# Optimization experiments

Measured on AMD Instinct MI355X. Metric: run time of the kernel, lower is better.

The kernel has to match this reference:

```python
import jax, jax.numpy as jnp
import numpy as np

B, IN_DIM, HID = 4096, 1024, 1024


def setup_inputs() -> dict:
    key = jax.random.key(0)
    ks = jax.random.split(key, 6)
    x_t = jax.random.normal(ks[0], (B, IN_DIM), dtype=jnp.float32)
    h_prev = jax.random.normal(ks[1], (B, HID), dtype=jnp.float32)
    c_prev = jax.random.normal(ks[2], (B, HID), dtype=jnp.float32)
    # stacked input-proj weights for gates (f, i, o, g): [4H, in_dim]
    U_w = jax.random.normal(ks[3], (4 * HID, IN_DIM), dtype=jnp.float32) * (1.0 / np.sqrt(IN_DIM))
    # biases: zeros except forget-gate bias = 1.0 (matches Uf.bias.fill_(1.0))
    U_b = jnp.concatenate([jnp.ones((HID,), jnp.float32), jnp.zeros((3 * HID,), jnp.float32)])
    # stacked hidden-proj weights (no bias): [4H, H]
    W_w = jax.random.normal(ks[4], (4 * HID, HID), dtype=jnp.float32) * (1.0 / np.sqrt(HID))
    return {"x_t": x_t, "h_prev": h_prev, "c_prev": c_prev,
            "U_w": U_w, "U_b": U_b, "W_w": W_w}


def reference(x_t, h_prev, c_prev, U_w, U_b, W_w):
    # two concatenated GEMMs covering all 8 original Linear layers
    pre = x_t @ U_w.T + U_b + h_prev @ W_w.T  # [B, 4H]
    f_pre, i_pre, o_pre, g_pre = jnp.split(pre, 4, axis=-1)
    f_t = jax.nn.sigmoid(f_pre)
    i_t = jax.nn.sigmoid(i_pre)
    o_t = jax.nn.sigmoid(o_pre)
    g_t = jnp.tanh(g_pre)
    c_t = f_t * c_prev + i_t * g_t
    h_t = o_t * jnp.tanh(c_t)
    return (h_t, c_t)
```

## Files before the change

### kernel.cpp

```cpp
#include <hip/hip_runtime.h>
#include <hip/hip_bf16.h>


#define BATCH 4096
#define HID   1024
#define KDIM  2048

#define BM 256
#define BN 256
#define BK 64
#define NITER (KDIM / (2 * BK))

typedef __bf16 bf16x8 __attribute__((ext_vector_type(8)));
typedef float  f32x4  __attribute__((ext_vector_type(4)));

__device__ __forceinline__ void async_load16(const void* g, void* l) {
    __builtin_amdgcn_global_load_lds(
        (const __attribute__((address_space(1))) void*)g,
        (__attribute__((address_space(3))) void*)l,
        16, 0, 0);
}

__device__ __forceinline__ float sigmoidf_(float v) {
    return 1.0f / (1.0f + __expf(-v));
}
__device__ __forceinline__ float tanhf_(float v) {
    return 1.0f - 2.0f / (__expf(2.0f * v) + 1.0f);
}

__global__ __launch_bounds__(256) void convert_kernel(
    const float* __restrict__ x, const float* __restrict__ h,
    const float* __restrict__ U, const float* __restrict__ W,
    __hip_bfloat16* __restrict__ Acat, __hip_bfloat16* __restrict__ Bcat)
{
    const int CH_PER_MAT = (4096 * KDIM) / 8;
    int idx = blockIdx.x * blockDim.x + threadIdx.x;
    bool isB = idx >= CH_PER_MAT;
    int c = isB ? (idx - CH_PER_MAT) : idx;
    int row  = c >> 8;
    int col  = (c & 255) << 3;
    int srow = row;
    if (isB) {
        int g  = (row >> 4) & 3;
        int j  = ((row >> 8) << 6) + (((row >> 6) & 3) << 4) + (row & 15);
        srow = g * 1024 + j;
    }
    const float* src;
    if (col < 1024) src = (isB ? U : x) + (size_t)srow * 1024 + col;
    else            src = (isB ? W : h) + (size_t)srow * 1024 + (col - 1024);
    float4 v0 = *(const float4*)(src);
    float4 v1 = *(const float4*)(src + 4);
    __hip_bfloat16 tmp[8];
    tmp[0] = __float2bfloat16(v0.x); tmp[1] = __float2bfloat16(v0.y);
    tmp[2] = __float2bfloat16(v0.z); tmp[3] = __float2bfloat16(v0.w);
    tmp[4] = __float2bfloat16(v1.x); tmp[5] = __float2bfloat16(v1.y);
    tmp[6] = __float2bfloat16(v1.z); tmp[7] = __float2bfloat16(v1.w);
    __hip_bfloat16* dst = (isB ? Bcat : Acat) + (size_t)row * KDIM + col;
    *(bf16x8*)dst = *(const bf16x8*)tmp;
}

__global__ __launch_bounds__(512, 1) void gemm_lstm_kernel(
    const __hip_bfloat16* __restrict__ A,
    const __hip_bfloat16* __restrict__ Bm,
    const float* __restrict__ Ub,
    const float* __restrict__ c_prev,
    float* __restrict__ out)
{
    __shared__ __align__(16) unsigned char smem[131072];

    const int tid  = threadIdx.x;
    const int lane = tid & 63;
    const int wid  = tid >> 6;
    const int wm   = wid >> 2;
    const int wn   = wid & 3;

    int wg  = blockIdx.x;
    const int xcd = wg & 7;
    const int i_  = wg >> 3;
    const int bm = ((xcd >> 1) << 2) + (i_ >> 3);
    const int bn = ((xcd & 1) << 3) + (i_ & 7);

    const __hip_bfloat16* Ab = A  + (size_t)bm * BM * KDIM;
    const __hip_bfloat16* Bb = Bm + (size_t)bn * BN * KDIM;

    const int frow = lane & 15;
    const int kq   = lane >> 4;
    const int esw  = (frow >> 1) & 7;
    const unsigned xs0 = (unsigned)((kq ^ esw) << 4);
    const unsigned xs1 = xs0 ^ 64u;
    const unsigned wmBase = (unsigned)wm * 16384u;
    const unsigned bnBase = (unsigned)(wn >> 1) * 16384u;
    const unsigned bnRow  = (unsigned)(wn & 1) * 64u;

    const int ch0 = tid,           ch1 = 512 + tid;
    const int sr0 = ch0 >> 3,      sr1 = ch1 >> 3;
    const int sc0 = ((ch0 & 7) ^ ((sr0 >> 1) & 7)) << 3;
    const int sc1 = ((ch1 & 7) ^ ((sr1 >> 1) & 7)) << 3;
    const size_t ga0 = (size_t)sr0 * KDIM + sc0;
    const size_t ga1 = (size_t)sr1 * KDIM + sc1;

    f32x4 acc[8][4] = {};
    bf16x8 arE[4], arO[4], brE[4], brO[4];

#define RD16(B) (*(const bf16x8*)(smem + (B)))
#define LDA4(SET, BUFB, MH, XS) do { \
    const unsigned _b = (BUFB) + wmBase; \
    SET[0] = RD16(_b + (unsigned)((MH)*64 +  0 + frow)*128u + (XS)); \
    SET[1] = RD16(_b + (unsigned)((MH)*64 + 16 + frow)*128u + (XS)); \
    SET[2] = RD16(_b + (unsigned)((MH)*64 + 32 + frow)*128u + (XS)); \
    SET[3] = RD16(_b + (unsigned)((MH)*64 + 48 + frow)*128u + (XS)); } while (0)
#define LDB4(SET, BUFB, XS) do { \
    const unsigned _b = (BUFB) + 32768u + bnBase; \
    SET[0] = RD16(_b + (bnRow +  0 + frow)*128u + (XS)); \
    SET[1] = RD16(_b + (bnRow + 16 + frow)*128u + (XS)); \
    SET[2] = RD16(_b + (bnRow + 32 + frow)*128u + (XS)); \
    SET[3] = RD16(_b + (bnRow + 48 + frow)*128u + (XS)); } while (0)
#define STG_A(TSRC, BUFB, H) do { \
    const unsigned _rg = (BUFB) + (H)*16384u; \
    const __hip_bfloat16* _s = Ab + (size_t)(H)*128*KDIM + (size_t)(TSRC)*64; \
    async_load16(_s + ga0, smem + _rg + (unsigned)ch0*16u); \
    async_load16(_s + ga1, smem + _rg + (unsigned)ch1*16u); } while (0)
#define STG_B(TSRC, BUFB, H) do { \
    const unsigned _rg = (BUFB) + 32768u + (H)*16384u; \
    const __hip_bfloat16* _s = Bb + (size_t)(H)*128*KDIM + (size_t)(TSRC)*64; \
    async_load16(_s + ga0, smem + _rg + (unsigned)ch0*16u); \
    async_load16(_s + ga1, smem + _rg + (unsigned)ch1*16u); } while (0)
#define MF16(ASET, BSET, MB) do { \
    __builtin_amdgcn_s_setprio(1); \
    _Pragma("unroll") for (int _m = 0; _m < 4; ++_m) \
    _Pragma("unroll") for (int _n = 0; _n < 4; ++_n) \
        acc[(MB)+_m][_n] = __builtin_amdgcn_mfma_f32_16x16x32_bf16( \
            ASET[_m], BSET[_n], acc[(MB)+_m][_n], 0, 0, 0); \
    __builtin_amdgcn_s_setprio(0); } while (0)
#define DRAIN_LGKM asm volatile("s_waitcnt lgkmcnt(0)" ::: "memory")
#define WAIT_VM4   asm volatile("s_waitcnt vmcnt(4)" ::: "memory")
#define PH_BAR __builtin_amdgcn_s_barrier()

    STG_B(0, 0u, 0); STG_B(0, 0u, 1);
    STG_A(0, 0u, 0); STG_A(0, 0u, 1);
    STG_B(1, 65536u, 0); STG_B(1, 65536u, 1);
    STG_A(1, 65536u, 0);
    asm volatile("s_waitcnt vmcnt(6)" ::: "memory");
    PH_BAR;
    LDA4(arE, 0u, 0, xs0); LDB4(brE, 0u, xs0);

#pragma unroll 1
    for (int i = 0; i < NITER; ++i) {
        const int tb = 2 * i + 1;
        const int tc = (2 * i + 2 < 32) ? 2 * i + 2 : 31;
        const int td = (2 * i + 3 < 32) ? 2 * i + 3 : 31;

        LDA4(arO, 0u, 0, xs1); LDB4(brO, 0u, xs1);
        STG_A(tb, 65536u, 1);
        MF16(arE, brE, 0);
        DRAIN_LGKM; PH_BAR;
        LDA4(arE, 0u, 1, xs0);
        STG_B(tc, 0u, 0);
        MF16(arO, brO, 0);
        PH_BAR;
        LDA4(arO, 0u, 1, xs1);
        STG_B(tc, 0u, 1);
        MF16(arE, brE, 4);
        DRAIN_LGKM; WAIT_VM4; PH_BAR;
        LDA4(arE, 65536u, 0, xs0); LDB4(brE, 65536u, xs0);
        STG_A(tc, 0u, 0);
        MF16(arO, brO, 4);
        PH_BAR;
        LDA4(arO, 65536u, 0, xs1); LDB4(brO, 65536u, xs1);
        STG_A(tc, 0u, 1);
        MF16(arE, brE, 0);
        DRAIN_LGKM; PH_BAR;
        LDA4(arE, 65536u, 1, xs0);
        STG_B(td, 65536u, 0);
        MF16(arO, brO, 0);
        PH_BAR;
        LDA4(arO, 65536u, 1, xs1);
        STG_B(td, 65536u, 1);
        MF16(arE, brE, 4);
        DRAIN_LGKM; WAIT_VM4; PH_BAR;
        LDA4(arE, 0u, 0, xs0); LDB4(brE, 0u, xs0);
        STG_A(td, 65536u, 0);
        MF16(arO, brO, 4);
        PH_BAR;
    }
#undef RD16
#undef LDA4
#undef LDB4
#undef STG_A
#undef STG_B
#undef MF16
#undef DRAIN_LGKM
#undef WAIT_VM4
#undef PH_BAR

    const int j = bn * 64 + wn * 16 + (lane & 15);
    const float bf_ = Ub[j];
    const float bi_ = Ub[1024 + j];
    const float bo_ = Ub[2048 + j];
    const float bg_ = Ub[3072 + j];
    const int row0 = bm * BM + wm * 128 + ((lane >> 4) << 2);

    float cp[8][4];
#pragma unroll
    for (int m = 0; m < 8; ++m)
#pragma unroll
        for (int r = 0; r < 4; ++r)
            cp[m][r] = c_prev[(size_t)(row0 + m * 16 + r) * HID + j];

#pragma unroll
    for (int m = 0; m < 8; ++m) {
#pragma unroll
        for (int r = 0; r < 4; ++r) {
            const int row = row0 + m * 16 + r;
            const float f  = sigmoidf_(acc[m][0][r] + bf_);
            const float it = sigmoidf_(acc[m][1][r] + bi_);
            const float o  = sigmoidf_(acc[m][2][r] + bo_);
            const float gg = tanhf_(acc[m][3][r] + bg_);
            const float cv = f * cp[m][r] + it * gg;
            const float hv = o * tanhf_(cv);
            out[(size_t)row * HID + j] = hv;
            out[(size_t)BATCH * HID + (size_t)row * HID + j] = cv;
        }
    }
}

extern "C" void kernel_launch(void* const* d_in, const int* in_sizes, int n_in,
                              void* d_out, int out_size, void* d_ws, size_t ws_size,
                              hipStream_t stream) {
    const float* x      = (const float*)d_in[0];
    const float* h_prev = (const float*)d_in[1];
    const float* c_prev = (const float*)d_in[2];
    const float* U_w    = (const float*)d_in[3];
    const float* U_b    = (const float*)d_in[4];
    const float* W_w    = (const float*)d_in[5];
    float* out = (float*)d_out;

    char* ws = (char*)d_ws;
    __hip_bfloat16* Acat = (__hip_bfloat16*)ws;
    __hip_bfloat16* Bcat = (__hip_bfloat16*)(ws + (16u << 20));

    convert_kernel<<<8192, 256, 0, stream>>>(x, h_prev, U_w, W_w, Acat, Bcat);
    gemm_lstm_kernel<<<256, 512, 0, stream>>>(Acat, Bcat, U_b, c_prev, out);
}
```

Measured before the change: 82.95 us.

## Replace register double-buffered fragments with barrier-separated load-then-compute phases

Drops the even/odd A-fragment register double buffering. Each phase now loads its fragments into a single temporary set, waits for the loads, then runs the MFMAs, so LDS reads no longer overlap with the previous phase's matrix math. This cuts register use and simplifies the schedule. The cost is roughly twice as many barriers and a full lgkmcnt drain before every MFMA group, which exposes LDS latency and is likely to slow the main loop.

```diff
diff --git a/kernel.cpp b/kernel.cpp
--- a/kernel.cpp
+++ b/kernel.cpp
@@ -100,7 +100,7 @@
     const size_t ga1 = (size_t)sr1 * KDIM + sc1;
 
     f32x4 acc[8][4] = {};
-    bf16x8 arE[4], arO[4], brE[4], brO[4];
+    bf16x8 arT[4], brE[4], brO[4];
 
 #define RD16(B) (*(const bf16x8*)(smem + (B)))
 #define LDA4(SET, BUFB, MH, XS) do { \
@@ -132,17 +132,17 @@
         acc[(MB)+_m][_n] = __builtin_amdgcn_mfma_f32_16x16x32_bf16( \
             ASET[_m], BSET[_n], acc[(MB)+_m][_n], 0, 0, 0); \
     __builtin_amdgcn_s_setprio(0); } while (0)
-#define DRAIN_LGKM asm volatile("s_waitcnt lgkmcnt(0)" ::: "memory")
-#define WAIT_VM4   asm volatile("s_waitcnt vmcnt(4)" ::: "memory")
-#define PH_BAR __builtin_amdgcn_s_barrier()
+#define LGKM0    asm volatile("s_waitcnt lgkmcnt(0)" ::: "memory")
+#define WAIT_VM4 asm volatile("s_waitcnt vmcnt(4)" ::: "memory")
+#define WAIT_VM6 asm volatile("s_waitcnt vmcnt(6)" ::: "memory")
+#define BAR      __builtin_amdgcn_s_barrier()
 
     STG_B(0, 0u, 0); STG_B(0, 0u, 1);
     STG_A(0, 0u, 0); STG_A(0, 0u, 1);
     STG_B(1, 65536u, 0); STG_B(1, 65536u, 1);
     STG_A(1, 65536u, 0);
-    asm volatile("s_waitcnt vmcnt(6)" ::: "memory");
-    PH_BAR;
-    LDA4(arE, 0u, 0, xs0); LDB4(brE, 0u, xs0);
+    WAIT_VM6;
+    BAR;
 
 #pragma unroll 1
     for (int i = 0; i < NITER; ++i) {
@@ -150,38 +150,48 @@
         const int tc = (2 * i + 2 < 32) ? 2 * i + 2 : 31;
         const int td = (2 * i + 3 < 32) ? 2 * i + 3 : 31;
 
-        LDA4(arO, 0u, 0, xs1); LDB4(brO, 0u, xs1);
+        LDA4(arT, 0u, 0, xs0); LDB4(brE, 0u, xs0);
         STG_A(tb, 65536u, 1);
-        MF16(arE, brE, 0);
-        DRAIN_LGKM; PH_BAR;
-        LDA4(arE, 0u, 1, xs0);
+        BAR; LGKM0;
+        MF16(arT, brE, 0);
+        BAR;
+        LDA4(arT, 0u, 0, xs1); LDB4(brO, 0u, xs1);
+        BAR; LGKM0;
+        MF16(arT, brO, 0);
+        BAR;
+        LDA4(arT, 0u, 1, xs0);
         STG_B(tc, 0u, 0);
-        MF16(arO, brO, 0);
-        PH_BAR;
-        LDA4(arO, 0u, 1, xs1);
+        BAR; LGKM0;
+        MF16(arT, brE, 4);
+        BAR;
+        LDA4(arT, 0u, 1, xs1);
         STG_B(tc, 0u, 1);
-        MF16(arE, brE, 4);
-        DRAIN_LGKM; WAIT_VM4; PH_BAR;
-        LDA4(arE, 65536u, 0, xs0); LDB4(brE, 65536u, xs0);
+        BAR; LGKM0;
+        MF16(arT, brO, 4);
+        WAIT_VM4;
+        BAR;
+        LDA4(arT, 65536u, 0, xs0); LDB4(brE, 65536u, xs0);
         STG_A(tc, 0u, 0);
-        MF16(arO, brO, 4);
-        PH_BAR;
-        LDA4(arO, 65536u, 0, xs1); LDB4(brO, 65536u, xs1);
+        BAR; LGKM0;
+        MF16(arT, brE, 0);
+        BAR;
+        LDA4(arT, 65536u, 0, xs1); LDB4(brO, 65536u, xs1);
         STG_A(tc, 0u, 1);
-        MF16(arE, brE, 0);
-        DRAIN_LGKM; PH_BAR;
-        LDA4(arE, 65536u, 1, xs0);
+        BAR; LGKM0;
+        MF16(arT, brO, 0);
+        BAR;
+        LDA4(arT, 65536u, 1, xs0);
         STG_B(td, 65536u, 0);
-        MF16(arO, brO, 0);
-        PH_BAR;
-        LDA4(arO, 65536u, 1, xs1);
+        BAR; LGKM0;
+        MF16(arT, brE, 4);
+        BAR;
+        LDA4(arT, 65536u, 1, xs1);
         STG_B(td, 65536u, 1);
-        MF16(arE, brE, 4);
-        DRAIN_LGKM; WAIT_VM4; PH_BAR;
-        LDA4(arE, 0u, 0, xs0); LDB4(brE, 0u, xs0);
         STG_A(td, 65536u, 0);
-        MF16(arO, brO, 4);
-        PH_BAR;
+        BAR; LGKM0;
+        MF16(arT, brO, 4);
+        WAIT_VM6;
+        BAR;
     }
 #undef RD16
 #undef LDA4
@@ -189,9 +199,10 @@
 #undef STG_A
 #undef STG_B
 #undef MF16
-#undef DRAIN_LGKM
+#undef LGKM0
 #undef WAIT_VM4
-#undef PH_BAR
+#undef WAIT_VM6
+#undef BAR
 
     const int j = bn * 64 + wn * 16 + (lane & 15);
     const float bf_ = Ub[j];
```

Result: slower. 85.94 us (+3.6%).

## Switch GEMM inner product from 16x16x32 to 32x32x16 bf16 MFMA tiles

Applied to the files above, without the earlier changes.

Replaces the 16x16x32 MFMA micro-tiles with 32x32x16 MFMA instructions, so each wave issues half as many MFMAs per stage with larger accumulators. The LDS fragment addressing and swizzle offsets are rewritten to match the 32-row operand layout. The epilogue uses lane shuffles to regroup the four gate values for each output element, and each half-wave writes either h or c. This aims to cut MFMA issue overhead and LDS read instructions, at the cost of shuffles and divergent stores in the epilogue.

```diff
diff --git a/kernel.cpp b/kernel.cpp
--- a/kernel.cpp
+++ b/kernel.cpp
@@ -12,7 +12,7 @@
 #define NITER (KDIM / (2 * BK))
 
 typedef __bf16 bf16x8 __attribute__((ext_vector_type(8)));
-typedef float  f32x4  __attribute__((ext_vector_type(4)));
+typedef float  f32x16 __attribute__((ext_vector_type(16)));
 
 __device__ __forceinline__ void async_load16(const void* g, void* l) {
     __builtin_amdgcn_global_load_lds(
@@ -83,14 +83,20 @@
     const __hip_bfloat16* Ab = A  + (size_t)bm * BM * KDIM;
     const __hip_bfloat16* Bb = Bm + (size_t)bn * BN * KDIM;
 
-    const int frow = lane & 15;
-    const int kq   = lane >> 4;
-    const int esw  = (frow >> 1) & 7;
-    const unsigned xs0 = (unsigned)((kq ^ esw) << 4);
-    const unsigned xs1 = xs0 ^ 64u;
+    const int l31 = lane & 31;
+    const int lhi = lane >> 5;
+    const int e7  = (l31 >> 1) & 7;
+    const unsigned lrow = (unsigned)l31 * 128u;
+    const unsigned cs0 = (unsigned)(((0 * 2 + lhi) ^ e7) << 4);
+    const unsigned cs1 = (unsigned)(((0 * 2 + 1 - lhi + lhi * 2) ^ e7) << 4);
+    const unsigned csA = (unsigned)(((0 + lhi) ^ e7) << 4);
+    const unsigned csB = (unsigned)(((2 + lhi) ^ e7) << 4);
+    const unsigned csC = (unsigned)(((4 + lhi) ^ e7) << 4);
+    const unsigned csD = (unsigned)(((6 + lhi) ^ e7) << 4);
+    (void)cs0; (void)cs1;
     const unsigned wmBase = (unsigned)wm * 16384u;
     const unsigned bnBase = (unsigned)(wn >> 1) * 16384u;
-    const unsigned bnRow  = (unsigned)(wn & 1) * 64u;
+    const unsigned bnRowB = (unsigned)(wn & 1) * 8192u;
 
     const int ch0 = tid,           ch1 = 512 + tid;
     const int sr0 = ch0 >> 3,      sr1 = ch1 >> 3;
@@ -99,22 +105,22 @@
     const size_t ga0 = (size_t)sr0 * KDIM + sc0;
     const size_t ga1 = (size_t)sr1 * KDIM + sc1;
 
-    f32x4 acc[8][4] = {};
-    bf16x8 arE[4], arO[4], brE[4], brO[4];
+    f32x16 acc[4][2] = {};
+    bf16x8 aE[4], aO[4], bE[4], bO[4];
 
 #define RD16(B) (*(const bf16x8*)(smem + (B)))
-#define LDA4(SET, BUFB, MH, XS) do { \
-    const unsigned _b = (BUFB) + wmBase; \
-    SET[0] = RD16(_b + (unsigned)((MH)*64 +  0 + frow)*128u + (XS)); \
-    SET[1] = RD16(_b + (unsigned)((MH)*64 + 16 + frow)*128u + (XS)); \
-    SET[2] = RD16(_b + (unsigned)((MH)*64 + 32 + frow)*128u + (XS)); \
-    SET[3] = RD16(_b + (unsigned)((MH)*64 + 48 + frow)*128u + (XS)); } while (0)
-#define LDB4(SET, BUFB, XS) do { \
-    const unsigned _b = (BUFB) + 32768u + bnBase; \
-    SET[0] = RD16(_b + (bnRow +  0 + frow)*128u + (XS)); \
-    SET[1] = RD16(_b + (bnRow + 16 + frow)*128u + (XS)); \
-    SET[2] = RD16(_b + (bnRow + 32 + frow)*128u + (XS)); \
-    SET[3] = RD16(_b + (bnRow + 48 + frow)*128u + (XS)); } while (0)
+#define LDA4(SET, BUFB, MH, KSL, KSH) do { \
+    const unsigned _b = (BUFB) + wmBase + (unsigned)(MH) * 8192u + lrow; \
+    SET[0] = RD16(_b +          (KSL)); \
+    SET[1] = RD16(_b +          (KSH)); \
+    SET[2] = RD16(_b + 4096u +  (KSL)); \
+    SET[3] = RD16(_b + 4096u +  (KSH)); } while (0)
+#define LDB4(SET, BUFB, KSL, KSH) do { \
+    const unsigned _b = (BUFB) + 32768u + bnBase + bnRowB + lrow; \
+    SET[0] = RD16(_b +          (KSL)); \
+    SET[1] = RD16(_b +          (KSH)); \
+    SET[2] = RD16(_b + 4096u +  (KSL)); \
+    SET[3] = RD16(_b + 4096u +  (KSH)); } while (0)
 #define STG_A(TSRC, BUFB, H) do { \
     const unsigned _rg = (BUFB) + (H)*16384u; \
     const __hip_bfloat16* _s = Ab + (size_t)(H)*128*KDIM + (size_t)(TSRC)*64; \
@@ -125,12 +131,16 @@
     const __hip_bfloat16* _s = Bb + (size_t)(H)*128*KDIM + (size_t)(TSRC)*64; \
     async_load16(_s + ga0, smem + _rg + (unsigned)ch0*16u); \
     async_load16(_s + ga1, smem + _rg + (unsigned)ch1*16u); } while (0)
-#define MF16(ASET, BSET, MB) do { \
+#define MF8(ASET, BSET, MB) do { \
     __builtin_amdgcn_s_setprio(1); \
-    _Pragma("unroll") for (int _m = 0; _m < 4; ++_m) \
-    _Pragma("unroll") for (int _n = 0; _n < 4; ++_n) \
-        acc[(MB)+_m][_n] = __builtin_amdgcn_mfma_f32_16x16x32_bf16( \
-            ASET[_m], BSET[_n], acc[(MB)+_m][_n], 0, 0, 0); \
+    acc[(MB)+0][0] = __builtin_amdgcn_mfma_f32_32x32x16_bf16(ASET[0], BSET[0], acc[(MB)+0][0], 0, 0, 0); \
+    acc[(MB)+0][1] = __builtin_amdgcn_mfma_f32_32x32x16_bf16(ASET[0], BSET[2], acc[(MB)+0][1], 0, 0, 0); \
+    acc[(MB)+1][0] = __builtin_amdgcn_mfma_f32_32x32x16_bf16(ASET[2], BSET[0], acc[(MB)+1][0], 0, 0, 0); \
+    acc[(MB)+1][1] = __builtin_amdgcn_mfma_f32_32x32x16_bf16(ASET[2], BSET[2], acc[(MB)+1][1], 0, 0, 0); \
+    acc[(MB)+0][0] = __builtin_amdgcn_mfma_f32_32x32x16_bf16(ASET[1], BSET[1], acc[(MB)+0][0], 0, 0, 0); \
+    acc[(MB)+0][1] = __builtin_amdgcn_mfma_f32_32x32x16_bf16(ASET[1], BSET[3], acc[(MB)+0][1], 0, 0, 0); \
+    acc[(MB)+1][0] = __builtin_amdgcn_mfma_f32_32x32x16_bf16(ASET[3], BSET[1], acc[(MB)+1][0], 0, 0, 0); \
+    acc[(MB)+1][1] = __builtin_amdgcn_mfma_f32_32x32x16_bf16(ASET[3], BSET[3], acc[(MB)+1][1], 0, 0, 0); \
     __builtin_amdgcn_s_setprio(0); } while (0)
 #define DRAIN_LGKM asm volatile("s_waitcnt lgkmcnt(0)" ::: "memory")
 #define WAIT_VM4   asm volatile("s_waitcnt vmcnt(4)" ::: "memory")
@@ -142,7 +152,7 @@
     STG_A(1, 65536u, 0);
     asm volatile("s_waitcnt vmcnt(6)" ::: "memory");
     PH_BAR;
-    LDA4(arE, 0u, 0, xs0); LDB4(brE, 0u, xs0);
+    LDA4(aE, 0u, 0, csA, csB); LDB4(bE, 0u, csA, csB);
 
 #pragma unroll 1
     for (int i = 0; i < NITER; ++i) {
@@ -150,37 +160,37 @@
         const int tc = (2 * i + 2 < 32) ? 2 * i + 2 : 31;
         const int td = (2 * i + 3 < 32) ? 2 * i + 3 : 31;
 
-        LDA4(arO, 0u, 0, xs1); LDB4(brO, 0u, xs1);
+        LDA4(aO, 0u, 0, csC, csD); LDB4(bO, 0u, csC, csD);
         STG_A(tb, 65536u, 1);
-        MF16(arE, brE, 0);
+        MF8(aE, bE, 0);
         DRAIN_LGKM; PH_BAR;
-        LDA4(arE, 0u, 1, xs0);
+        LDA4(aE, 0u, 1, csA, csB);
         STG_B(tc, 0u, 0);
-        MF16(arO, brO, 0);
-        PH_BAR;
-        LDA4(arO, 0u, 1, xs1);
+        MF8(aO, bO, 0);
+        PH_BAR;
+        LDA4(aO, 0u, 1, csC, csD);
         STG_B(tc, 0u, 1);
-        MF16(arE, brE, 4);
+        MF8(aE, bE, 2);
         DRAIN_LGKM; WAIT_VM4; PH_BAR;
-        LDA4(arE, 65536u, 0, xs0); LDB4(brE, 65536u, xs0);
+        LDA4(aE, 65536u, 0, csA, csB); LDB4(bE, 65536u, csA, csB);
         STG_A(tc, 0u, 0);
-        MF16(arO, brO, 4);
-        PH_BAR;
-        LDA4(arO, 65536u, 0, xs1); LDB4(brO, 65536u, xs1);
+        MF8(aO, bO, 2);
+        PH_BAR;
+        LDA4(aO, 65536u, 0, csC, csD); LDB4(bO, 65536u, csC, csD);
         STG_A(tc, 0u, 1);
-        MF16(arE, brE, 0);
+        MF8(aE, bE, 0);
         DRAIN_LGKM; PH_BAR;
-        LDA4(arE, 65536u, 1, xs0);
+        LDA4(aE, 65536u, 1, csA, csB);
         STG_B(td, 65536u, 0);
-        MF16(arO, brO, 0);
-        PH_BAR;
-        LDA4(arO, 65536u, 1, xs1);
+        MF8(aO, bO, 0);
+        PH_BAR;
+        LDA4(aO, 65536u, 1, csC, csD);
         STG_B(td, 65536u, 1);
-        MF16(arE, brE, 4);
+        MF8(aE, bE, 2);
         DRAIN_LGKM; WAIT_VM4; PH_BAR;
-        LDA4(arE, 0u, 0, xs0); LDB4(brE, 0u, xs0);
+        LDA4(aE, 0u, 0, csA, csB); LDB4(bE, 0u, csA, csB);
         STG_A(td, 65536u, 0);
-        MF16(arO, brO, 4);
+        MF8(aO, bO, 2);
         PH_BAR;
     }
 #undef RD16
@@ -188,38 +198,41 @@
 #undef LDB4
 #undef STG_A
 #undef STG_B
-#undef MF16
+#undef MF8
 #undef DRAIN_LGKM
 #undef WAIT_VM4
 #undef PH_BAR
 
-    const int j = bn * 64 + wn * 16 + (lane & 15);
-    const float bf_ = Ub[j];
-    const float bi_ = Ub[1024 + j];
-    const float bo_ = Ub[2048 + j];
-    const float bg_ = Ub[3072 + j];
-    const int row0 = bm * BM + wm * 128 + ((lane >> 4) << 2);
-
-    float cp[8][4];
+    const int cc = l31 & 15;
+    const int hi = (l31 >> 4) & 1;
+    const int j = bn * 64 + wn * 16 + cc;
+    const float b0 = Ub[j];
+    const float b1 = Ub[1024 + j];
+    const float b2 = Ub[2048 + j];
+    const float b3 = Ub[3072 + j];
+    const int row0 = bm * BM + wm * 128 + (lhi << 2);
+
 #pragma unroll
-    for (int m = 0; m < 8; ++m)
+    for (int m = 0; m < 4; ++m) {
 #pragma unroll
-        for (int r = 0; r < 4; ++r)
-            cp[m][r] = c_prev[(size_t)(row0 + m * 16 + r) * HID + j];
-
-#pragma unroll
-    for (int m = 0; m < 8; ++m) {
-#pragma unroll
-        for (int r = 0; r < 4; ++r) {
-            const int row = row0 + m * 16 + r;
-            const float f  = sigmoidf_(acc[m][0][r] + bf_);
-            const float it = sigmoidf_(acc[m][1][r] + bi_);
-            const float o  = sigmoidf_(acc[m][2][r] + bo_);
-            const float gg = tanhf_(acc[m][3][r] + bg_);
-            const float cv = f * cp[m][r] + it * gg;
-            const float hv = o * tanhf_(cv);
-            out[(size_t)row * HID + j] = hv;
-            out[(size_t)BATCH * HID + (size_t)row * HID + j] = cv;
+        for (int reg = 0; reg < 16; ++reg) {
+            const int row = row0 + m * 32 + (reg & 3) + ((reg >> 2) << 3);
+            const float pa = acc[m][0][reg];
+            const float pb = acc[m][1][reg];
+            const float xa = __shfl_xor(pa, 16);
+            const float xb = __shfl_xor(pb, 16);
+            const float fpre = hi ? xa : pa;
+            const float ipre = hi ? pa : xa;
+            const float opre = hi ? xb : pb;
+            const float gpre = hi ? pb : xb;
+            const float cp = c_prev[(size_t)row * HID + j];
+            const float f  = sigmoidf_(fpre + b0);
+            const float it = sigmoidf_(ipre + b1);
+            const float o  = sigmoidf_(opre + b2);
+            const float gg = tanhf_(gpre + b3);
+            const float cv = f * cp + it * gg;
+            if (hi) out[(size_t)BATCH * HID + (size_t)row * HID + j] = cv;
+            else    out[(size_t)row * HID + j] = o * tanhf_(cv);
         }
     }
 }
```

New measurement: 103.3 us. 1.24x slower.
